# Kernel tuning notes

Hardware: AMD Instinct MI355X
Metric: run time of the kernel (lower is better)

## Reference

```python
import jax, jax.numpy as jnp
import numpy as np

B, N, D, H = 2, 2048, 1024, 16
DH = D // H  # 64


def setup_inputs() -> dict:
    key = jax.random.key(0)
    ks = jax.random.split(key, 5)
    s = 1.0 / np.sqrt(D)
    x = jax.random.normal(ks[0], (B, N, D), jnp.float32)
    # per-head kqv Linear weights, stacked: [H, D, 3*DH]
    Wkqv = jax.random.normal(ks[1], (H, D, 3 * DH), jnp.float32) * s
    bkqv = jax.random.normal(ks[2], (H, 3 * DH), jnp.float32) * 0.02
    Wo = jax.random.normal(ks[3], (D, D), jnp.float32) * s
    bo = jax.random.normal(ks[4], (D,), jnp.float32) * 0.02
    return {"x": x, "Wkqv": Wkqv, "bkqv": bkqv, "Wo": Wo, "bo": bo}


def reference(x, Wkqv, bkqv, Wo, bo):
    Bs, Ns, Ds = x.shape
    Hs = Wkqv.shape[0]
    dh = Wkqv.shape[-1] // 3
    # all heads' kqv projections at once: [B, H, N, 3*dh]
    kqv_out = jnp.einsum('bnd,hde->bhne', x, Wkqv) + bkqv[None, :, None, :]
    # original splits in order (k, q, v)
    k, q, v = jnp.split(kqv_out, 3, axis=-1)
    # NOTE: original computes attention_scores(k, q) = k @ q^T (swapped vs standard)
    A = jnp.einsum('bhnd,bhmd->bhnm', k, q) / jnp.sqrt(jnp.asarray(dh, x.dtype))
    mask = jnp.tril(jnp.ones((Ns, Ns), dtype=bool))
    A = jnp.where(mask[None, None], A, -jnp.inf)
    alpha = jax.nn.softmax(A, axis=-1)
    sa = jnp.einsum('bhnm,bhmd->bhnd', alpha, v)  # [B, H, N, dh]
    # concat heads along feature dim (head0..headH-1 order)
    sa = sa.transpose(0, 2, 1, 3).reshape(Bs, Ns, Hs * dh)
    return sa @ Wo + bo
```

## Files before the change

### kernel.cpp

```cpp
#include <hip/hip_runtime.h>
#include <hip/hip_bf16.h>
#include <cstdint>
#include <cstddef>

typedef __bf16 bf16x8 __attribute__((ext_vector_type(8)));
typedef __bf16 bf16x4 __attribute__((ext_vector_type(4)));
typedef float  f32x4  __attribute__((ext_vector_type(4)));

constexpr int Bc = 2, Nc = 2048, Dc = 1024, Hc = 16, DHc = 64;
constexpr int BN = Bc * Nc;
constexpr int E3 = 3 * DHc;
constexpr int BH = Bc * Hc;
constexpr int NK = Hc * E3;

__device__ __forceinline__ f32x4 mfma16(bf16x8 a, bf16x8 b, f32x4 c) {
  return __builtin_amdgcn_mfma_f32_16x16x32_bf16(a, b, c, 0, 0, 0);
}

__device__ __forceinline__ void gload16(const __bf16* g, __bf16* l) {
  __builtin_amdgcn_global_load_lds((const __attribute__((address_space(1))) void*)g,
                                   (__attribute__((address_space(3))) void*)l,
                                   16, 0, 0);
}

__device__ __forceinline__ float fexp2(float x) {
  return __builtin_amdgcn_exp2f(x);
}

constexpr int TP = 68;
__global__ __launch_bounds__(256) void cvt_all_kernel(
    const float* __restrict__ x,    __bf16* __restrict__ xb,
    const float* __restrict__ Wkqv, __bf16* __restrict__ wkt,
    const float* __restrict__ Wo,   __bf16* __restrict__ wot) {
  __shared__ __bf16 T[64][TP];
  const int blk = blockIdx.x;
  const int tid = threadIdx.x;
  if (blk < 4096) {
    int i = (blk * 256 + tid) * 4;
    float4 v = *(const float4*)(x + i);
    xb[i + 0] = (__bf16)v.x;
    xb[i + 1] = (__bf16)v.y;
    xb[i + 2] = (__bf16)v.z;
    xb[i + 3] = (__bf16)v.w;
    return;
  }
  const float* src;
  __bf16* dst;
  int R, C, c0, r0;
  size_t sbase;
  if (blk < 4096 + 768) {
    const int local = blk - 4096;
    R = Dc; C = E3;
    c0 = (local % 3) * 64;
    r0 = ((local / 3) & 15) * 64;
    sbase = (size_t)(local / 48) * R * C;
    src = Wkqv; dst = wkt;
  } else {
    const int local = blk - (4096 + 768);
    R = Dc; C = Dc;
    c0 = (local & 15) * 64;
    r0 = (local >> 4) * 64;
    sbase = 0;
    src = Wo; dst = wot;
  }
#pragma unroll
  for (int it = 0; it < 4; ++it) {
    int g = tid + it * 256;
    int r = g >> 4, c4 = (g & 15) * 4;
    float4 v = *(const float4*)&src[sbase + (size_t)(r0 + r) * C + c0 + c4];
    T[c4 + 0][r] = (__bf16)v.x;
    T[c4 + 1][r] = (__bf16)v.y;
    T[c4 + 2][r] = (__bf16)v.z;
    T[c4 + 3][r] = (__bf16)v.w;
  }
  __syncthreads();
#pragma unroll
  for (int it = 0; it < 2; ++it) {
    int g = tid + it * 256;
    int c = g >> 3, ch = (g & 7) * 8;
    bf16x4 u0 = *(const bf16x4*)&T[c][ch];
    bf16x4 u1 = *(const bf16x4*)&T[c][ch + 4];
    __bf16* dp = &dst[sbase + (size_t)(c0 + c) * R + r0 + ch];
    *(bf16x4*)dp = u0;
    *(bf16x4*)(dp + 4) = u1;
  }
}

__launch_bounds__(256)
__global__ void kqv_gemm_kernel(const __bf16* __restrict__ xb,
                                const __bf16* __restrict__ wkt,
                                const float* __restrict__ bkqv,
                                __bf16* __restrict__ kqv,
                                __bf16* __restrict__ vT) {
  const int mt = blockIdx.x;
  const int h  = blockIdx.y;
  __shared__ __align__(16) __bf16 Al[2][128][64];
  __shared__ __align__(16) __bf16 Bl[2][192][64];
  const int tid  = threadIdx.x;
  const int lane = tid & 63;
  const int w    = tid >> 6;
  const int fr   = lane & 15, fq = lane >> 4;
  const int fq4  = fq * 4;
  const int WR   = (w >> 1) * 64, WC = (w & 1) * 96;
  const int sr   = tid >> 3;
  const int sc8  = ((tid & 7) ^ (sr & 7)) * 8;
  const int wb   = (w << 3);
  const int m0   = mt * 128;
  const __bf16* wth = wkt + (size_t)h * E3 * Dc;

  auto STAGE = [&](int buf, int k0) {
#pragma unroll
    for (int j = 0; j < 4; ++j)
      gload16(&xb[(size_t)(m0 + j * 32 + sr) * Dc + k0 + sc8], &Al[buf][j * 32 + wb][0]);
#pragma unroll
    for (int j = 0; j < 6; ++j)
      gload16(&wth[(size_t)(j * 32 + sr) * Dc + k0 + sc8], &Bl[buf][j * 32 + wb][0]);
  };

  f32x4 acc[4][6] = {};
  STAGE(0, 0);
  int cur = 0;
  for (int t = 0; t < 16; ++t) {
    if (t < 15) {
      STAGE(cur ^ 1, (t + 1) * 64);
      asm volatile("s_waitcnt vmcnt(10)" ::: "memory");
    } else {
      asm volatile("s_waitcnt vmcnt(0)" ::: "memory");
    }
    asm volatile("s_barrier" ::: "memory");
    const char* Ab = (const char*)&Al[cur][0][0];
    const char* Bb = (const char*)&Bl[cur][0][0];
#pragma unroll
    for (int ks = 0; ks < 2; ++ks) {
      bf16x8 a_[4], b_[6];
#pragma unroll
      for (int mr = 0; mr < 4; ++mr) {
        int r = WR + mr * 16 + fr;
        a_[mr] = *(const bf16x8*)(Ab + r * 128 + ((ks * 64 + fq * 16) ^ ((r & 7) << 4)));
      }
#pragma unroll
      for (int nc = 0; nc < 6; ++nc) {
        int r = WC + nc * 16 + fr;
        b_[nc] = *(const bf16x8*)(Bb + r * 128 + ((ks * 64 + fq * 16) ^ ((r & 7) << 4)));
      }
#pragma unroll
      for (int mr = 0; mr < 4; ++mr)
#pragma unroll
        for (int nc = 0; nc < 6; ++nc)
          acc[mr][nc] = mfma16(a_[mr], b_[nc], acc[mr][nc]);
    }
    asm volatile("s_barrier" ::: "memory");
    cur ^= 1;
  }

  const int b = m0 >> 11;
#pragma unroll
  for (int nc = 0; nc < 6; ++nc) {
    const int eb = WC + nc * 16;
    const float bias = bkqv[h * E3 + eb + fr];
    if (eb < 64) {
      const float sc = 0.125f * 1.44269504088896f;
      const int el = eb + fr;
#pragma unroll
      for (int mr = 0; mr < 4; ++mr) {
        int nn0 = (m0 & (Nc - 1)) + WR + mr * 16 + fq4;
        bf16x4 v4;
#pragma unroll
        for (int i = 0; i < 4; ++i) v4[i] = (__bf16)((acc[mr][nc][i] + bias) * sc);
        *(bf16x4*)&kqv[((size_t)((b * Hc + h) * DHc + el)) * Nc + nn0] = v4;
      }
    } else if (eb < 128) {
      const int e = (eb - 64) + fr;
      __bf16* dst = kqv + (size_t)BH * Nc * DHc +
                    ((size_t)(b * Hc + h)) * Nc * DHc + e;
#pragma unroll
      for (int mr = 0; mr < 4; ++mr)
#pragma unroll
        for (int i = 0; i < 4; ++i) {
          int n = (m0 & (Nc - 1)) + WR + mr * 16 + fq4 + i;
          dst[(size_t)n * DHc] = (__bf16)(acc[mr][nc][i] + bias);
        }
    } else {
      const int el = eb - 128 + fr;
#pragma unroll
      for (int mr = 0; mr < 4; ++mr) {
        int nn0 = (m0 & (Nc - 1)) + WR + mr * 16 + fq4;
        bf16x4 v4;
#pragma unroll
        for (int i = 0; i < 4; ++i) v4[i] = (__bf16)(acc[mr][nc][i] + bias);
        *(bf16x4*)&vT[((size_t)((b * Hc + h) * DHc + el)) * Nc + nn0] = v4;
      }
    }
  }
}

__launch_bounds__(256)
__global__ void attn_kernel(const __bf16* __restrict__ kT,
                            const __bf16* __restrict__ qb,
                            const __bf16* __restrict__ vT,
                            __bf16* __restrict__ sab) {
  const int bx = blockIdx.x;
  const int by = blockIdx.y;
  const int bh   = 4 * (bx & 7) + (by >> 3);
  const int pair = (bx >> 3) * 8 + (by & 7);
  __shared__ __align__(16) __bf16 KqL[2][64][64];
  __shared__ __align__(16) __bf16 VtL[2][64][64];
  __shared__ __align__(16) __bf16 Pl[4][16][64];
  const int tid  = threadIdx.x;
  const int lane = tid & 63;
  const int w    = tid >> 6;
  const int fr   = lane & 15, fq = lane >> 4;
  const int fq4  = fq * 4;
  const int key  = (fr & 7) << 4;
  const int off0 = (fq * 16) ^ key;
  const int off1 = (fq * 16 + 64) ^ key;
  const __bf16* kth = kT + (size_t)bh * DHc * Nc;
  const __bf16* qbh = qb + (size_t)bh * Nc * DHc;
  const __bf16* vth = vT + (size_t)bh * DHc * Nc;
  const int b = bh >> 4, h = bh & 15;
  char* Pw = (char*)&Pl[w][0][0];

  const int sch  = (tid & 7);
  const int r_s0 = tid >> 3;
  const int r_s1 = r_s0 + 32;
  const int swb0 = r_s0 * 128 + ((sch * 16) ^ ((r_s0 & 7) << 4));
  const int swb1 = r_s1 * 128 + ((sch * 16) ^ ((r_s1 & 7) << 4));

  for (int ph = 0; ph < 2; ++ph) {
    const int qt   = ph ? (31 - pair) : pair;
    const int n0   = qt * 64 + w * 16;
    const int ncol = n0 + fr;

    bf16x8 bq0, bq1;
#pragma unroll
    for (int j = 0; j < 8; ++j) {
      bq0[j] = kth[(size_t)(8 * fq + j) * Nc + n0 + fr];
      bq1[j] = kth[(size_t)(32 + 8 * fq + j) * Nc + n0 + fr];
    }

    float l_run = 0.f;
    f32x4 acc[4] = {};

    __syncthreads();
    {
      bf16x8 k0a = *(const bf16x8*)&qbh[(size_t)r_s0 * DHc + sch * 8];
      bf16x8 k0b = *(const bf16x8*)&qbh[(size_t)r_s1 * DHc + sch * 8];
      bf16x8 v0a = *(const bf16x8*)&vth[(size_t)r_s0 * Nc + sch * 8];
      bf16x8 v0b = *(const bf16x8*)&vth[(size_t)r_s1 * Nc + sch * 8];
      *(bf16x8*)((char*)&KqL[0][0][0] + swb0) = k0a;
      *(bf16x8*)((char*)&KqL[0][0][0] + swb1) = k0b;
      *(bf16x8*)((char*)&VtL[0][0][0] + swb0) = v0a;
      *(bf16x8*)((char*)&VtL[0][0][0] + swb1) = v0b;
    }
    __syncthreads();

    int cur = 0;
    for (int t = 0; t <= qt; ++t) {
      bf16x8 nk0, nk1, nv0, nv1;
      const bool more = (t < qt);
      if (more) {
        const int v1 = (t + 1) * 64;
        nk0 = *(const bf16x8*)&qbh[(size_t)(v1 + r_s0) * DHc + sch * 8];
        nk1 = *(const bf16x8*)&qbh[(size_t)(v1 + r_s1) * DHc + sch * 8];
        nv0 = *(const bf16x8*)&vth[(size_t)r_s0 * Nc + v1 + sch * 8];
        nv1 = *(const bf16x8*)&vth[(size_t)r_s1 * Nc + v1 + sch * 8];
      }

      const char* Kqb = (const char*)&KqL[cur][0][0];
      const char* Vtb = (const char*)&VtL[cur][0][0];

      f32x4 s[4];
      __builtin_amdgcn_s_setprio(1);
#pragma unroll
      for (int c = 0; c < 4; ++c) {
        const char* rp = Kqb + (c * 16 + fr) * 128;
        bf16x8 t0 = *(const bf16x8*)(rp + off0);
        bf16x8 t1 = *(const bf16x8*)(rp + off1);
        f32x4 z = {};
        z = mfma16(t0, bq0, z);
        z = mfma16(t1, bq1, z);
        s[c] = z;
      }
      __builtin_amdgcn_s_setprio(0);

      if (t == qt) {
        const int thr = ncol - t * 64;
#pragma unroll
        for (int c = 0; c < 4; ++c)
#pragma unroll
          for (int i = 0; i < 4; ++i) {
            float pv = fexp2(s[c][i]);
            s[c][i] = (c * 16 + fq4 + i > thr) ? 0.f : pv;
          }
      } else {
#pragma unroll
        for (int c = 0; c < 4; ++c)
#pragma unroll
          for (int i = 0; i < 4; ++i) s[c][i] = fexp2(s[c][i]);
      }
      float cs0 = (s[0][0] + s[0][1]) + (s[0][2] + s[0][3]);
      float cs1 = (s[1][0] + s[1][1]) + (s[1][2] + s[1][3]);
      float cs2 = (s[2][0] + s[2][1]) + (s[2][2] + s[2][3]);
      float cs3 = (s[3][0] + s[3][1]) + (s[3][2] + s[3][3]);
      l_run += (cs0 + cs1) + (cs2 + cs3);

#pragma unroll
      for (int c = 0; c < 4; ++c) {
        bf16x4 p4;
#pragma unroll
        for (int i = 0; i < 4; ++i) p4[i] = (__bf16)s[c][i];
        *(bf16x4*)(Pw + fr * 128 + ((c * 32 + fq * 8) ^ key)) = p4;
      }
      asm volatile("s_waitcnt lgkmcnt(0)" ::: "memory");
      __builtin_amdgcn_sched_barrier(0);

      __builtin_amdgcn_s_setprio(1);
      bf16x8 ap0 = *(const bf16x8*)(Pw + fr * 128 + off0);
      bf16x8 ap1 = *(const bf16x8*)(Pw + fr * 128 + off1);
#pragma unroll
      for (int d = 0; d < 4; ++d) {
        const char* vp = Vtb + (d * 16 + fr) * 128;
        bf16x8 bv0 = *(const bf16x8*)(vp + off0);
        bf16x8 bv1 = *(const bf16x8*)(vp + off1);
        acc[d] = mfma16(ap0, bv0, acc[d]);
        acc[d] = mfma16(ap1, bv1, acc[d]);
      }
      __builtin_amdgcn_s_setprio(0);

      if (more) {
        char* Kn = (char*)&KqL[cur ^ 1][0][0];
        char* Vn = (char*)&VtL[cur ^ 1][0][0];
        *(bf16x8*)(Kn + swb0) = nk0;
        *(bf16x8*)(Kn + swb1) = nk1;
        *(bf16x8*)(Vn + swb0) = nv0;
        *(bf16x8*)(Vn + swb1) = nv1;
      }
      __syncthreads();
      cur ^= 1;
    }

    l_run += __shfl_xor(l_run, 16);
    l_run += __shfl_xor(l_run, 32);
    float linv[4];
#pragma unroll
    for (int ii = 0; ii < 4; ++ii) linv[ii] = 1.0f / __shfl(l_run, fq4 + ii);
#pragma unroll
    for (int d = 0; d < 4; ++d)
#pragma unroll
      for (int ii = 0; ii < 4; ++ii) {
        int n  = n0 + fq4 + ii;
        int dd = d * 16 + fr;
        sab[((size_t)(b * Nc + n)) * Dc + h * DHc + dd] = (__bf16)(acc[d][ii] * linv[ii]);
      }
  }
}

__launch_bounds__(256)
__global__ void out_gemm_kernel(const __bf16* __restrict__ sab,
                                const __bf16* __restrict__ wot,
                                const float* __restrict__ bo,
                                float* __restrict__ out) {
  const int mt = blockIdx.x;
  const int nt = blockIdx.y;
  __shared__ __align__(16) __bf16 Al[2][64][64];
  __shared__ __align__(16) __bf16 Bl[2][128][64];
  const int tid  = threadIdx.x;
  const int lane = tid & 63;
  const int w    = tid >> 6;
  const int fr   = lane & 15, fq = lane >> 4;
  const int fq4  = fq * 4;
  const int WR   = (w >> 1) * 32, WC = (w & 1) * 64;
  const int sr   = tid >> 3;
  const int sc8  = ((tid & 7) ^ (sr & 7)) * 8;
  const int wb   = (w << 3);
  const int m0   = mt * 64, n0 = nt * 128;

  auto STAGE = [&](int buf, int k0) {
#pragma unroll
    for (int j = 0; j < 2; ++j)
      gload16(&sab[(size_t)(m0 + j * 32 + sr) * Dc + k0 + sc8], &Al[buf][j * 32 + wb][0]);
#pragma unroll
    for (int j = 0; j < 4; ++j)
      gload16(&wot[(size_t)(n0 + j * 32 + sr) * Dc + k0 + sc8], &Bl[buf][j * 32 + wb][0]);
  };

  f32x4 acc[2][4] = {};
  STAGE(0, 0);
  int cur = 0;
  for (int t = 0; t < 16; ++t) {
    if (t < 15) {
      STAGE(cur ^ 1, (t + 1) * 64);
      asm volatile("s_waitcnt vmcnt(6)" ::: "memory");
    } else {
      asm volatile("s_waitcnt vmcnt(0)" ::: "memory");
    }
    asm volatile("s_barrier" ::: "memory");
    const char* Ab = (const char*)&Al[cur][0][0];
    const char* Bb = (const char*)&Bl[cur][0][0];
#pragma unroll
    for (int ks = 0; ks < 2; ++ks) {
      bf16x8 a_[2], b_[4];
#pragma unroll
      for (int mr = 0; mr < 2; ++mr) {
        int r = WR + mr * 16 + fr;
        a_[mr] = *(const bf16x8*)(Ab + r * 128 + ((ks * 64 + fq * 16) ^ ((r & 7) << 4)));
      }
#pragma unroll
      for (int nc = 0; nc < 4; ++nc) {
        int r = WC + nc * 16 + fr;
        b_[nc] = *(const bf16x8*)(Bb + r * 128 + ((ks * 64 + fq * 16) ^ ((r & 7) << 4)));
      }
#pragma unroll
      for (int mr = 0; mr < 2; ++mr)
#pragma unroll
        for (int nc = 0; nc < 4; ++nc)
          acc[mr][nc] = mfma16(a_[mr], b_[nc], acc[mr][nc]);
    }
    asm volatile("s_barrier" ::: "memory");
    cur ^= 1;
  }
#pragma unroll
  for (int mr = 0; mr < 2; ++mr)
#pragma unroll
    for (int nc = 0; nc < 4; ++nc)
#pragma unroll
      for (int i = 0; i < 4; ++i) {
        int m = m0 + WR + mr * 16 + fq4 + i;
        int e = n0 + WC + nc * 16 + fr;
        out[(size_t)m * Dc + e] = acc[mr][nc][i] + bo[e];
      }
}

extern "C" void kernel_launch(void* const* d_in, const int* in_sizes, int n_in,
                              void* d_out, int out_size, void* d_ws, size_t ws_size,
                              hipStream_t stream) {
  const float* x    = (const float*)d_in[0];
  const float* Wkqv = (const float*)d_in[1];
  const float* bkqv = (const float*)d_in[2];
  const float* Wo   = (const float*)d_in[3];
  const float* bo   = (const float*)d_in[4];
  float* out = (float*)d_out;

  __bf16* xb   = (__bf16*)d_ws;
  __bf16* wkt  = xb  + (size_t)BN * Dc;
  __bf16* wot  = wkt + (size_t)NK * Dc;
  __bf16* kqv  = wot + (size_t)Dc * Dc;
  __bf16* kTb  = kqv;
  __bf16* qbuf = kqv + (size_t)BH * Nc * DHc;
  __bf16* vTb  = kqv + 2 * (size_t)BH * Nc * DHc;
  __bf16* sab  = kqv + 3 * (size_t)BH * Nc * DHc;

  cvt_all_kernel<<<4096 + 768 + 256, 256, 0, stream>>>(x, xb, Wkqv, wkt, Wo, wot);

  kqv_gemm_kernel<<<dim3(BN / 128, Hc), 256, 0, stream>>>(xb, wkt, bkqv, kqv, vTb);

  attn_kernel<<<dim3(16, BH), 256, 0, stream>>>(kTb, qbuf, vTb, sab);

  out_gemm_kernel<<<dim3(BN / 64, Dc / 128), 256, 0, stream>>>(sab, wot, bo, out);
}
```

Baseline: 94.35 us.

## Software-pipeline PV matmul one tile behind QK to overlap with exp

Restructures the attention inner loop so the P·V MFMAs for the previous key tile run right after the current tile's score MFMAs. The exp/softmax work can then overlap with matrix work, and the explicit lgkmcnt wait and sched barrier between the P store and reload go away. P is double-buffered and V is triple-buffered in LDS to keep the lagged tile alive, with a drain step after the loop. This costs extra LDS and registers and could lower occupancy.

```diff
diff --git a/kernel.cpp b/kernel.cpp
--- a/kernel.cpp
+++ b/kernel.cpp
@@ -204,8 +204,8 @@
   const int bh   = 4 * (bx & 7) + (by >> 3);
   const int pair = (bx >> 3) * 8 + (by & 7);
   __shared__ __align__(16) __bf16 KqL[2][64][64];
-  __shared__ __align__(16) __bf16 VtL[2][64][64];
-  __shared__ __align__(16) __bf16 Pl[4][16][64];
+  __shared__ __align__(16) __bf16 VtL[3][64][64];
+  __shared__ __align__(16) __bf16 Pl[2][4][16][64];
   const int tid  = threadIdx.x;
   const int lane = tid & 63;
   const int w    = tid >> 6;
@@ -218,7 +218,6 @@
   const __bf16* qbh = qb + (size_t)bh * Nc * DHc;
   const __bf16* vth = vT + (size_t)bh * DHc * Nc;
   const int b = bh >> 4, h = bh & 15;
-  char* Pw = (char*)&Pl[w][0][0];
 
   const int sch  = (tid & 7);
   const int r_s0 = tid >> 3;
@@ -254,7 +253,7 @@
     }
     __syncthreads();
 
-    int cur = 0;
+    int kcur = 0;
     for (int t = 0; t <= qt; ++t) {
       bf16x8 nk0, nk1, nv0, nv1;
       const bool more = (t < qt);
@@ -266,8 +265,7 @@
         nv1 = *(const bf16x8*)&vth[(size_t)r_s1 * Nc + v1 + sch * 8];
       }
 
-      const char* Kqb = (const char*)&KqL[cur][0][0];
-      const char* Vtb = (const char*)&VtL[cur][0][0];
+      const char* Kqb = (const char*)&KqL[kcur][0][0];
 
       f32x4 s[4];
       __builtin_amdgcn_s_setprio(1);
@@ -281,6 +279,20 @@
         z = mfma16(t1, bq1, z);
         s[c] = z;
       }
+      if (t > 0) {
+        const char* Pp = (const char*)&Pl[(t - 1) & 1][w][0][0];
+        const char* Vp = (const char*)&VtL[(t - 1) % 3][0][0];
+        bf16x8 ap0 = *(const bf16x8*)(Pp + fr * 128 + off0);
+        bf16x8 ap1 = *(const bf16x8*)(Pp + fr * 128 + off1);
+#pragma unroll
+        for (int d = 0; d < 4; ++d) {
+          const char* vp = Vp + (d * 16 + fr) * 128;
+          bf16x8 bv0 = *(const bf16x8*)(vp + off0);
+          bf16x8 bv1 = *(const bf16x8*)(vp + off1);
+          acc[d] = mfma16(ap0, bv0, acc[d]);
+          acc[d] = mfma16(ap1, bv1, acc[d]);
+        }
+      }
       __builtin_amdgcn_s_setprio(0);
 
       if (t == qt) {
@@ -304,39 +316,44 @@
       float cs3 = (s[3][0] + s[3][1]) + (s[3][2] + s[3][3]);
       l_run += (cs0 + cs1) + (cs2 + cs3);
 
-#pragma unroll
-      for (int c = 0; c < 4; ++c) {
-        bf16x4 p4;
-#pragma unroll
-        for (int i = 0; i < 4; ++i) p4[i] = (__bf16)s[c][i];
-        *(bf16x4*)(Pw + fr * 128 + ((c * 32 + fq * 8) ^ key)) = p4;
-      }
-      asm volatile("s_waitcnt lgkmcnt(0)" ::: "memory");
-      __builtin_amdgcn_sched_barrier(0);
-
+      {
+        char* Pc = (char*)&Pl[t & 1][w][0][0];
+#pragma unroll
+        for (int c = 0; c < 4; ++c) {
+          bf16x4 p4;
+#pragma unroll
+          for (int i = 0; i < 4; ++i) p4[i] = (__bf16)s[c][i];
+          *(bf16x4*)(Pc + fr * 128 + ((c * 32 + fq * 8) ^ key)) = p4;
+        }
+      }
+
+      if (more) {
+        char* Kn = (char*)&KqL[kcur ^ 1][0][0];
+        char* Vn = (char*)&VtL[(t + 1) % 3][0][0];
+        *(bf16x8*)(Kn + swb0) = nk0;
+        *(bf16x8*)(Kn + swb1) = nk1;
+        *(bf16x8*)(Vn + swb0) = nv0;
+        *(bf16x8*)(Vn + swb1) = nv1;
+      }
+      __syncthreads();
+      kcur ^= 1;
+    }
+
+    {
+      const char* Pp = (const char*)&Pl[qt & 1][w][0][0];
+      const char* Vp = (const char*)&VtL[qt % 3][0][0];
+      bf16x8 ap0 = *(const bf16x8*)(Pp + fr * 128 + off0);
+      bf16x8 ap1 = *(const bf16x8*)(Pp + fr * 128 + off1);
       __builtin_amdgcn_s_setprio(1);
-      bf16x8 ap0 = *(const bf16x8*)(Pw + fr * 128 + off0);
-      bf16x8 ap1 = *(const bf16x8*)(Pw + fr * 128 + off1);
 #pragma unroll
       for (int d = 0; d < 4; ++d) {
-        const char* vp = Vtb + (d * 16 + fr) * 128;
+        const char* vp = Vp + (d * 16 + fr) * 128;
         bf16x8 bv0 = *(const bf16x8*)(vp + off0);
         bf16x8 bv1 = *(const bf16x8*)(vp + off1);
         acc[d] = mfma16(ap0, bv0, acc[d]);
         acc[d] = mfma16(ap1, bv1, acc[d]);
       }
       __builtin_amdgcn_s_setprio(0);
-
-      if (more) {
-        char* Kn = (char*)&KqL[cur ^ 1][0][0];
-        char* Vn = (char*)&VtL[cur ^ 1][0][0];
-        *(bf16x8*)(Kn + swb0) = nk0;
-        *(bf16x8*)(Kn + swb1) = nk1;
-        *(bf16x8*)(Vn + swb0) = nv0;
-        *(bf16x8*)(Vn + swb1) = nv1;
-      }
-      __syncthreads();
-      cur ^= 1;
     }
 
     l_run += __shfl_xor(l_run, 16);
```

Measured after the change: 96.78 us. 2.6% more time.
